# Optimization experiments

Hardware: AMD Instinct MI355X
Metric: run time of the kernel (lower is better)

The kernel has to match this reference:

```python
import jax, jax.numpy as jnp
import numpy as np

V = 500000        # total elements
S = 50000         # num samples (segments)
D = 128           # input = hidden = output size


def setup_inputs() -> dict:
    key = jax.random.key(0)
    k1, k2, k3, k4, k5 = jax.random.split(key, 5)
    scale = 1.0 / np.sqrt(D)
    return {
        "element_embeddings": jax.random.normal(k1, (V, D), dtype=jnp.float32),
        "element_to_sample_map": jnp.sort(jax.random.randint(k2, (V,), 0, S)),
        "num_samples": S,
        "Wq": jax.random.normal(k3, (D, D), dtype=jnp.float32) * scale,
        "Wk": jax.random.normal(k4, (D, D), dtype=jnp.float32) * scale,
        "Wo": jax.random.normal(k5, (D, D), dtype=jnp.float32) * scale,
    }


def reference(element_embeddings, element_to_sample_map, num_samples, Wq, Wk, Wo):
    x = element_embeddings                    # [V, D]
    idx = element_to_sample_map               # [V] int

    # --- query summarizer: linear projection + segment mean ---
    q_elem = x @ Wq.T                          # [V, H]
    q_sum = jax.ops.segment_sum(q_elem, idx, num_segments=num_samples)   # [S, H]
    counts = jax.ops.segment_sum(jnp.ones((x.shape[0],), x.dtype), idx,
                                 num_segments=num_samples)               # [S]
    queries = q_sum / jnp.maximum(counts, 1.0)[:, None]                  # [S, H]

    # --- attention scores: gather query per element, dot with key ---
    keys = x @ Wk.T                            # [V, H]
    queries_all = queries[idx]                 # [V, H] gather
    scores = jnp.einsum('vh,vh->v', queries_all, keys)                   # [V]

    # --- segment softmax (exp of scatter_log_softmax, eps=0) ---
    seg_max = jax.ops.segment_max(scores, idx, num_segments=num_samples) # [S]
    shifted = scores - seg_max[idx]
    e = jnp.exp(shifted)
    denom = jax.ops.segment_sum(e, idx, num_segments=num_samples)        # [S]
    probs = e / denom[idx]                                               # [V]

    # --- weighted scatter-sum of output projections ---
    out_elem = (x @ Wo.T) * probs[:, None]     # [V, D_out]
    return jax.ops.segment_sum(out_elem, idx, num_segments=num_samples)  # [S, D_out]
```

## Files before the change

kernel.cpp:

```cpp
#include <hip/hip_runtime.h>
#include <math.h>

#define D 128
#define RPW 64
#define WPB 4
#define RPB (RPW * WPB)

__global__ void k_prep(const float* __restrict__ Wq, const float* __restrict__ Wk,
                       const float* __restrict__ Wo, float* __restrict__ M,
                       float* __restrict__ WoT) {
  int j = blockIdx.x, k = threadIdx.x;
  float acc = 0.f;
#pragma unroll 8
  for (int i = 0; i < D; ++i) acc = fmaf(Wq[i * D + j], Wk[i * D + k], acc);
  M[j * D + k] = acc;
  WoT[j * D + k] = Wo[k * D + j];
}

__global__ void k_zero(float4* __restrict__ p, long long nf4) {
  long long i = (long long)blockIdx.x * blockDim.x + threadIdx.x;
  long long st = (long long)gridDim.x * blockDim.x;
  float4 z = make_float4(0.f, 0.f, 0.f, 0.f);
  for (; i < nf4; i += st) p[i] = z;
}

template <int PASS>
__global__ __launch_bounds__(256) void k_segsum(
    const float* __restrict__ x, const int* __restrict__ idx,
    const float* __restrict__ t, float* __restrict__ gout,
    float* __restrict__ gden, int V) {
  const int lane = threadIdx.x & 63;
  const int wave = threadIdx.x >> 6;
  const int r0 = blockIdx.x * RPB + wave * RPW;
  if (r0 >= V) return;

  const int myIdx = idx[min(r0 + lane, V - 1)];
  const int prevIdx = __shfl_up(myIdx, 1);
  const unsigned long long chg = __ballot(lane > 0 && myIdx != prevIdx);

  const float* xw = x + (size_t)r0 * D + lane * 2;
  float2 acc = make_float2(0.f, 0.f);
  float dacc = 0.f;
  int curSeg = __shfl(myIdx, 0);
  int runStart = 0;
  float2 t2 = make_float2(0.f, 0.f);
  if (PASS == 2) t2 = *(const float2*)(t + (size_t)curSeg * D + lane * 2);

#pragma unroll
  for (int c = 0; c < RPW / 8; ++c) {
    float2 xr[8];
#pragma unroll
    for (int j = 0; j < 8; ++j) {
      int rr = min(r0 + c * 8 + j, V - 1) - r0;
      xr[j] = *(const float2*)(xw + (size_t)rr * D);
    }
#pragma unroll
    for (int j = 0; j < 8; ++j) {
      const int i = c * 8 + j;
      const bool valid = (r0 + i) < V;
      if (i > 0 && ((chg >> i) & 1ull)) {
        float* gp = gout + (size_t)curSeg * D + lane * 2;
        if (runStart > 0) {
          gp[0] = acc.x;
          gp[1] = acc.y;
          if (lane == 0) gden[curSeg] = dacc;
        } else {
          unsafeAtomicAdd(gp + 0, acc.x);
          unsafeAtomicAdd(gp + 1, acc.y);
          if (lane == 0) unsafeAtomicAdd(gden + curSeg, dacc);
        }
        acc = make_float2(0.f, 0.f);
        dacc = 0.f;
        curSeg = __shfl(myIdx, i);
        runStart = i;
        if (PASS == 2) t2 = *(const float2*)(t + (size_t)curSeg * D + lane * 2);
      }
      float w;
      if (PASS == 1) {
        w = valid ? 1.f : 0.f;
      } else {
        float p = t2.x * xr[j].x + t2.y * xr[j].y;
        p += __shfl_xor(p, 32);
        p += __shfl_xor(p, 16);
        p += __shfl_xor(p, 8);
        p += __shfl_xor(p, 4);
        p += __shfl_xor(p, 2);
        p += __shfl_xor(p, 1);
        w = valid ? __expf(p) : 0.f;
      }
      acc.x = fmaf(w, xr[j].x, acc.x);
      acc.y = fmaf(w, xr[j].y, acc.y);
      dacc += w;
    }
  }
  float* gp = gout + (size_t)curSeg * D + lane * 2;
  unsafeAtomicAdd(gp + 0, acc.x);
  unsafeAtomicAdd(gp + 1, acc.y);
  if (lane == 0) unsafeAtomicAdd(gden + curSeg, dacc);
}

template <int MODE>
__global__ void k_rowmat4(const float* __restrict__ in, const float* __restrict__ B,
                          float* __restrict__ out, int S,
                          const float* __restrict__ den) {
  __shared__ float Bl[D * D];
  for (int i = threadIdx.x; i < D * D / 4; i += (int)blockDim.x)
    ((float4*)Bl)[i] = ((const float4*)B)[i];
  __syncthreads();
  int t = blockIdx.x * blockDim.x + threadIdx.x;
  int g = t & 31;
  int s0 = (t >> 5) * 4;
  if (s0 >= S) return;
  int nr = S - s0;
  nr = nr > 4 ? 4 : nr;
  float4 a0 = make_float4(0, 0, 0, 0), a1 = a0, a2 = a0, a3 = a0;
  const float4* r0 = (const float4*)(in + (size_t)s0 * D);
  const float4* r1 = (const float4*)(in + (size_t)(s0 + 1) * D);
  const float4* r2 = (const float4*)(in + (size_t)(s0 + 2) * D);
  const float4* r3 = (const float4*)(in + (size_t)(s0 + 3) * D);
#pragma unroll 4
  for (int j4 = 0; j4 < D / 4; ++j4) {
    float4 b0 = *(const float4*)(Bl + (j4 * 4 + 0) * D + g * 4);
    float4 b1 = *(const float4*)(Bl + (j4 * 4 + 1) * D + g * 4);
    float4 b2 = *(const float4*)(Bl + (j4 * 4 + 2) * D + g * 4);
    float4 b3 = *(const float4*)(Bl + (j4 * 4 + 3) * D + g * 4);
#define ROWFMA(ar, rr)                                                   \
    {                                                                    \
      float4 m = rr[j4];                                                 \
      ar.x = fmaf(m.x, b0.x, ar.x); ar.y = fmaf(m.x, b0.y, ar.y);        \
      ar.z = fmaf(m.x, b0.z, ar.z); ar.w = fmaf(m.x, b0.w, ar.w);        \
      ar.x = fmaf(m.y, b1.x, ar.x); ar.y = fmaf(m.y, b1.y, ar.y);        \
      ar.z = fmaf(m.y, b1.z, ar.z); ar.w = fmaf(m.y, b1.w, ar.w);        \
      ar.x = fmaf(m.z, b2.x, ar.x); ar.y = fmaf(m.z, b2.y, ar.y);        \
      ar.z = fmaf(m.z, b2.z, ar.z); ar.w = fmaf(m.z, b2.w, ar.w);        \
      ar.x = fmaf(m.w, b3.x, ar.x); ar.y = fmaf(m.w, b3.y, ar.y);        \
      ar.z = fmaf(m.w, b3.z, ar.z); ar.w = fmaf(m.w, b3.w, ar.w);        \
    }
    ROWFMA(a0, r0);
    if (nr > 1) ROWFMA(a1, r1);
    if (nr > 2) ROWFMA(a2, r2);
    if (nr > 3) ROWFMA(a3, r3);
#undef ROWFMA
  }
  float sc[4];
#pragma unroll
  for (int k = 0; k < 4; ++k) {
    int s = s0 + (k < nr ? k : 0);
    float dn = den[s];
    if (MODE == 0) sc[k] = 1.f / fmaxf(dn, 1.f);
    else sc[k] = (dn > 0.f) ? 1.f / dn : 0.f;
  }
  a0.x *= sc[0]; a0.y *= sc[0]; a0.z *= sc[0]; a0.w *= sc[0];
  a1.x *= sc[1]; a1.y *= sc[1]; a1.z *= sc[1]; a1.w *= sc[1];
  a2.x *= sc[2]; a2.y *= sc[2]; a2.z *= sc[2]; a2.w *= sc[2];
  a3.x *= sc[3]; a3.y *= sc[3]; a3.z *= sc[3]; a3.w *= sc[3];
  *(float4*)(out + (size_t)s0 * D + g * 4) = a0;
  if (nr > 1) *(float4*)(out + (size_t)(s0 + 1) * D + g * 4) = a1;
  if (nr > 2) *(float4*)(out + (size_t)(s0 + 2) * D + g * 4) = a2;
  if (nr > 3) *(float4*)(out + (size_t)(s0 + 3) * D + g * 4) = a3;
}

extern "C" void kernel_launch(void* const* d_in, const int* in_sizes, int n_in,
                              void* d_out, int out_size, void* d_ws, size_t ws_size,
                              hipStream_t stream) {
  const float* x = (const float*)d_in[0];
  const int* idx = (const int*)d_in[1];
  const float* Wq = (const float*)d_in[3];
  const float* Wk = (const float*)d_in[4];
  const float* Wo = (const float*)d_in[5];
  float* out = (float*)d_out;
  const int V = in_sizes[1];
  const int S = out_size / D;

  char* ws = (char*)d_ws;
  float* M = (float*)(ws + 0);
  float* WoT = (float*)(ws + 65536);
  size_t base = 131072;
  float* qsum = (float*)(ws + base);
  float* ysum = qsum + (size_t)S * D;
  float* cnt = ysum + (size_t)S * D;
  float* den = cnt + S;
  long long zf4 = ((long long)S * (2 * D + 2)) / 4;
  size_t tbase = (base + (size_t)S * (2 * D + 2) * 4 + 255) & ~(size_t)255;
  float* t = (float*)(ws + tbase);

  const int NT = (V + RPB - 1) / RPB;
  const int rmBlocks = ((S + 3) / 4 * 32 + 255) / 256;

  hipLaunchKernelGGL(k_prep, dim3(D), dim3(D), 0, stream, Wq, Wk, Wo, M, WoT);
  hipLaunchKernelGGL(k_zero, dim3(2048), dim3(256), 0, stream, (float4*)qsum, zf4);
  hipLaunchKernelGGL((k_segsum<1>), dim3(NT), dim3(256), 0, stream, x, idx,
                     (const float*)nullptr, qsum, cnt, V);
  hipLaunchKernelGGL((k_rowmat4<0>), dim3(rmBlocks), dim3(256), 0, stream, qsum, M, t, S, cnt);
  hipLaunchKernelGGL((k_segsum<2>), dim3(NT), dim3(256), 0, stream, x, idx, t, ysum, den, V);
  hipLaunchKernelGGL((k_rowmat4<1>), dim3(rmBlocks), dim3(256), 0, stream, ysum, WoT, out, S, den);
}
```

Measured before the change: 298.1 us.

## Fuse all stages into one persistent kernel with software grid barriers

Replaces six kernel launches with a single persistent kernel sized from occupancy. Its phases (zero/prep, pass-1 segment sum, query projection, pass-2 weighted sum, output projection) are separated by an atomic sense-reversing grid barrier. The aim is to remove launch gaps and tail effects between the small stages. The segment passes now use 32-row waves in grid-strided tiles, and the rowmat phase stages B in 32-row chunks through a smaller shared buffer. The software barrier relies on all blocks being co-resident, which plain launches do not guarantee, and it adds spin overhead and smaller per-wave work.

```diff
diff --git a/kernel.cpp b/kernel.cpp
--- a/kernel.cpp
+++ b/kernel.cpp
@@ -2,162 +2,243 @@
 #include <math.h>
 
 #define D 128
-#define RPW 64
-#define WPB 4
-#define RPB (RPW * WPB)
-
-__global__ void k_prep(const float* __restrict__ Wq, const float* __restrict__ Wk,
-                       const float* __restrict__ Wo, float* __restrict__ M,
-                       float* __restrict__ WoT) {
-  int j = blockIdx.x, k = threadIdx.x;
-  float acc = 0.f;
-#pragma unroll 8
-  for (int i = 0; i < D; ++i) acc = fmaf(Wq[i * D + j], Wk[i * D + k], acc);
-  M[j * D + k] = acc;
-  WoT[j * D + k] = Wo[k * D + j];
-}
-
-__global__ void k_zero(float4* __restrict__ p, long long nf4) {
-  long long i = (long long)blockIdx.x * blockDim.x + threadIdx.x;
-  long long st = (long long)gridDim.x * blockDim.x;
-  float4 z = make_float4(0.f, 0.f, 0.f, 0.f);
-  for (; i < nf4; i += st) p[i] = z;
+#define TPB 512
+#define WPB 8
+#define RPWAVE 32
+#define RPT (WPB * RPWAVE)
+
+__device__ __forceinline__ void grid_barrier(int* gcount, int* gsense, int nb,
+                                             int* bsense) {
+  __syncthreads();
+  if (threadIdx.x == 0) {
+    int s = 1 - *bsense;
+    *bsense = s;
+    __threadfence();
+    int arrived = __hip_atomic_fetch_add(gcount, 1, __ATOMIC_ACQ_REL,
+                                         __HIP_MEMORY_SCOPE_AGENT);
+    if (arrived == nb - 1) {
+      __hip_atomic_store(gcount, 0, __ATOMIC_RELAXED, __HIP_MEMORY_SCOPE_AGENT);
+      __hip_atomic_store(gsense, s, __ATOMIC_RELEASE, __HIP_MEMORY_SCOPE_AGENT);
+    } else {
+      while (__hip_atomic_load(gsense, __ATOMIC_ACQUIRE,
+                               __HIP_MEMORY_SCOPE_AGENT) != s)
+        __builtin_amdgcn_s_sleep(8);
+    }
+  }
+  __syncthreads();
 }
 
 template <int PASS>
-__global__ __launch_bounds__(256) void k_segsum(
-    const float* __restrict__ x, const int* __restrict__ idx,
-    const float* __restrict__ t, float* __restrict__ gout,
-    float* __restrict__ gden, int V) {
+__device__ __forceinline__ void seg_pass(const float* __restrict__ x,
+                                         const int* __restrict__ idx,
+                                         const float* __restrict__ t,
+                                         float* __restrict__ gout,
+                                         float* __restrict__ gden, int V) {
   const int lane = threadIdx.x & 63;
   const int wave = threadIdx.x >> 6;
-  const int r0 = blockIdx.x * RPB + wave * RPW;
-  if (r0 >= V) return;
-
-  const int myIdx = idx[min(r0 + lane, V - 1)];
-  const int prevIdx = __shfl_up(myIdx, 1);
-  const unsigned long long chg = __ballot(lane > 0 && myIdx != prevIdx);
-
-  const float* xw = x + (size_t)r0 * D + lane * 2;
-  float2 acc = make_float2(0.f, 0.f);
-  float dacc = 0.f;
-  int curSeg = __shfl(myIdx, 0);
-  int runStart = 0;
-  float2 t2 = make_float2(0.f, 0.f);
-  if (PASS == 2) t2 = *(const float2*)(t + (size_t)curSeg * D + lane * 2);
-
-#pragma unroll
-  for (int c = 0; c < RPW / 8; ++c) {
-    float2 xr[8];
-#pragma unroll
-    for (int j = 0; j < 8; ++j) {
-      int rr = min(r0 + c * 8 + j, V - 1) - r0;
-      xr[j] = *(const float2*)(xw + (size_t)rr * D);
-    }
-#pragma unroll
-    for (int j = 0; j < 8; ++j) {
-      const int i = c * 8 + j;
-      const bool valid = (r0 + i) < V;
-      if (i > 0 && ((chg >> i) & 1ull)) {
-        float* gp = gout + (size_t)curSeg * D + lane * 2;
-        if (runStart > 0) {
-          gp[0] = acc.x;
-          gp[1] = acc.y;
-          if (lane == 0) gden[curSeg] = dacc;
+  const int NT = (V + RPT - 1) / RPT;
+  for (int tile = blockIdx.x; tile < NT; tile += gridDim.x) {
+    const int r0 = tile * RPT + wave * RPWAVE;
+    if (r0 >= V) continue;
+    int rowIdx = idx[min(r0 + (lane & 31), V - 1)];
+    int prev = __shfl_up(rowIdx, 1);
+    unsigned long long chg = __ballot(lane > 0 && lane < 32 && rowIdx != prev);
+
+    float2 acc = make_float2(0.f, 0.f);
+    float dacc = 0.f;
+    int curSeg = __shfl(rowIdx, 0);
+    int runStart = 0;
+    float2 t2 = make_float2(0.f, 0.f);
+    if (PASS == 2) t2 = *(const float2*)(t + (size_t)curSeg * D + lane * 2);
+
+#pragma unroll
+    for (int c = 0; c < RPWAVE / 8; ++c) {
+      float2 xr[8];
+#pragma unroll
+      for (int j = 0; j < 8; ++j) {
+        int row = r0 + c * 8 + j;
+        row = row < V ? row : V - 1;
+        xr[j] = *(const float2*)(x + (size_t)row * D + lane * 2);
+      }
+#pragma unroll
+      for (int j = 0; j < 8; ++j) {
+        const int i = c * 8 + j;
+        const bool valid = (r0 + i) < V;
+        if (i > 0 && ((chg >> i) & 1ull)) {
+          float* gp = gout + (size_t)curSeg * D + lane * 2;
+          if (runStart > 0) {
+            gp[0] = acc.x;
+            gp[1] = acc.y;
+            if (lane == 0) gden[curSeg] = dacc;
+          } else {
+            unsafeAtomicAdd(gp + 0, acc.x);
+            unsafeAtomicAdd(gp + 1, acc.y);
+            if (lane == 0) unsafeAtomicAdd(gden + curSeg, dacc);
+          }
+          acc = make_float2(0.f, 0.f);
+          dacc = 0.f;
+          curSeg = __shfl(rowIdx, i);
+          runStart = i;
+          if (PASS == 2) t2 = *(const float2*)(t + (size_t)curSeg * D + lane * 2);
+        }
+        float w;
+        if (PASS == 1) {
+          w = valid ? 1.f : 0.f;
         } else {
-          unsafeAtomicAdd(gp + 0, acc.x);
-          unsafeAtomicAdd(gp + 1, acc.y);
-          if (lane == 0) unsafeAtomicAdd(gden + curSeg, dacc);
-        }
-        acc = make_float2(0.f, 0.f);
-        dacc = 0.f;
-        curSeg = __shfl(myIdx, i);
-        runStart = i;
-        if (PASS == 2) t2 = *(const float2*)(t + (size_t)curSeg * D + lane * 2);
-      }
-      float w;
-      if (PASS == 1) {
-        w = valid ? 1.f : 0.f;
-      } else {
-        float p = t2.x * xr[j].x + t2.y * xr[j].y;
-        p += __shfl_xor(p, 32);
-        p += __shfl_xor(p, 16);
-        p += __shfl_xor(p, 8);
-        p += __shfl_xor(p, 4);
-        p += __shfl_xor(p, 2);
-        p += __shfl_xor(p, 1);
-        w = valid ? __expf(p) : 0.f;
-      }
-      acc.x = fmaf(w, xr[j].x, acc.x);
-      acc.y = fmaf(w, xr[j].y, acc.y);
-      dacc += w;
-    }
-  }
-  float* gp = gout + (size_t)curSeg * D + lane * 2;
-  unsafeAtomicAdd(gp + 0, acc.x);
-  unsafeAtomicAdd(gp + 1, acc.y);
-  if (lane == 0) unsafeAtomicAdd(gden + curSeg, dacc);
-}
+          float p = t2.x * xr[j].x + t2.y * xr[j].y;
+          p += __shfl_xor(p, 32);
+          p += __shfl_xor(p, 16);
+          p += __shfl_xor(p, 8);
+          p += __shfl_xor(p, 4);
+          p += __shfl_xor(p, 2);
+          p += __shfl_xor(p, 1);
+          w = valid ? __expf(p) : 0.f;
+        }
+        acc.x = fmaf(w, xr[j].x, acc.x);
+        acc.y = fmaf(w, xr[j].y, acc.y);
+        dacc += w;
+      }
+    }
+    float* gp = gout + (size_t)curSeg * D + lane * 2;
+    unsafeAtomicAdd(gp + 0, acc.x);
+    unsafeAtomicAdd(gp + 1, acc.y);
+    if (lane == 0) unsafeAtomicAdd(gden + curSeg, dacc);
+  }
+}
+
+#define FMA16(ar, m, b0, b1, b2, b3)                                   \
+  {                                                                    \
+    ar.x = fmaf(m.x, b0.x, ar.x); ar.y = fmaf(m.x, b0.y, ar.y);        \
+    ar.z = fmaf(m.x, b0.z, ar.z); ar.w = fmaf(m.x, b0.w, ar.w);        \
+    ar.x = fmaf(m.y, b1.x, ar.x); ar.y = fmaf(m.y, b1.y, ar.y);        \
+    ar.z = fmaf(m.y, b1.z, ar.z); ar.w = fmaf(m.y, b1.w, ar.w);        \
+    ar.x = fmaf(m.z, b2.x, ar.x); ar.y = fmaf(m.z, b2.y, ar.y);        \
+    ar.z = fmaf(m.z, b2.z, ar.z); ar.w = fmaf(m.z, b2.w, ar.w);        \
+    ar.x = fmaf(m.w, b3.x, ar.x); ar.y = fmaf(m.w, b3.y, ar.y);        \
+    ar.z = fmaf(m.w, b3.z, ar.z); ar.w = fmaf(m.w, b3.w, ar.w);        \
+  }
 
 template <int MODE>
-__global__ void k_rowmat4(const float* __restrict__ in, const float* __restrict__ B,
-                          float* __restrict__ out, int S,
-                          const float* __restrict__ den) {
-  __shared__ float Bl[D * D];
-  for (int i = threadIdx.x; i < D * D / 4; i += (int)blockDim.x)
-    ((float4*)Bl)[i] = ((const float4*)B)[i];
-  __syncthreads();
-  int t = blockIdx.x * blockDim.x + threadIdx.x;
-  int g = t & 31;
-  int s0 = (t >> 5) * 4;
-  if (s0 >= S) return;
-  int nr = S - s0;
-  nr = nr > 4 ? 4 : nr;
-  float4 a0 = make_float4(0, 0, 0, 0), a1 = a0, a2 = a0, a3 = a0;
-  const float4* r0 = (const float4*)(in + (size_t)s0 * D);
-  const float4* r1 = (const float4*)(in + (size_t)(s0 + 1) * D);
-  const float4* r2 = (const float4*)(in + (size_t)(s0 + 2) * D);
-  const float4* r3 = (const float4*)(in + (size_t)(s0 + 3) * D);
-#pragma unroll 4
-  for (int j4 = 0; j4 < D / 4; ++j4) {
-    float4 b0 = *(const float4*)(Bl + (j4 * 4 + 0) * D + g * 4);
-    float4 b1 = *(const float4*)(Bl + (j4 * 4 + 1) * D + g * 4);
-    float4 b2 = *(const float4*)(Bl + (j4 * 4 + 2) * D + g * 4);
-    float4 b3 = *(const float4*)(Bl + (j4 * 4 + 3) * D + g * 4);
-#define ROWFMA(ar, rr)                                                   \
-    {                                                                    \
-      float4 m = rr[j4];                                                 \
-      ar.x = fmaf(m.x, b0.x, ar.x); ar.y = fmaf(m.x, b0.y, ar.y);        \
-      ar.z = fmaf(m.x, b0.z, ar.z); ar.w = fmaf(m.x, b0.w, ar.w);        \
-      ar.x = fmaf(m.y, b1.x, ar.x); ar.y = fmaf(m.y, b1.y, ar.y);        \
-      ar.z = fmaf(m.y, b1.z, ar.z); ar.w = fmaf(m.y, b1.w, ar.w);        \
-      ar.x = fmaf(m.z, b2.x, ar.x); ar.y = fmaf(m.z, b2.y, ar.y);        \
-      ar.z = fmaf(m.z, b2.z, ar.z); ar.w = fmaf(m.z, b2.w, ar.w);        \
-      ar.x = fmaf(m.w, b3.x, ar.x); ar.y = fmaf(m.w, b3.y, ar.y);        \
-      ar.z = fmaf(m.w, b3.z, ar.z); ar.w = fmaf(m.w, b3.w, ar.w);        \
-    }
-    ROWFMA(a0, r0);
-    if (nr > 1) ROWFMA(a1, r1);
-    if (nr > 2) ROWFMA(a2, r2);
-    if (nr > 3) ROWFMA(a3, r3);
-#undef ROWFMA
-  }
-  float sc[4];
-#pragma unroll
-  for (int k = 0; k < 4; ++k) {
-    int s = s0 + (k < nr ? k : 0);
-    float dn = den[s];
-    if (MODE == 0) sc[k] = 1.f / fmaxf(dn, 1.f);
-    else sc[k] = (dn > 0.f) ? 1.f / dn : 0.f;
-  }
-  a0.x *= sc[0]; a0.y *= sc[0]; a0.z *= sc[0]; a0.w *= sc[0];
-  a1.x *= sc[1]; a1.y *= sc[1]; a1.z *= sc[1]; a1.w *= sc[1];
-  a2.x *= sc[2]; a2.y *= sc[2]; a2.z *= sc[2]; a2.w *= sc[2];
-  a3.x *= sc[3]; a3.y *= sc[3]; a3.z *= sc[3]; a3.w *= sc[3];
-  *(float4*)(out + (size_t)s0 * D + g * 4) = a0;
-  if (nr > 1) *(float4*)(out + (size_t)(s0 + 1) * D + g * 4) = a1;
-  if (nr > 2) *(float4*)(out + (size_t)(s0 + 2) * D + g * 4) = a2;
-  if (nr > 3) *(float4*)(out + (size_t)(s0 + 3) * D + g * 4) = a3;
+__device__ __forceinline__ void rowmat_phase(const float* __restrict__ in,
+                                             const float* __restrict__ B,
+                                             float* __restrict__ outp,
+                                             const float* __restrict__ scale_src,
+                                             int S, float* Bl) {
+  const int tid = threadIdx.x;
+  const int g = tid & 31;
+  const int gl = tid >> 5;
+  const int NG = (S + 127) / 128;
+  for (int bt = blockIdx.x; bt < NG; bt += gridDim.x) {
+    const int gid0 = bt * 32 + gl;
+    const int gid1 = bt * 32 + 16 + gl;
+    float4 accA[4], accB[4];
+#pragma unroll
+    for (int r = 0; r < 4; ++r) {
+      accA[r] = make_float4(0.f, 0.f, 0.f, 0.f);
+      accB[r] = make_float4(0.f, 0.f, 0.f, 0.f);
+    }
+#pragma unroll
+    for (int c = 0; c < 4; ++c) {
+      __syncthreads();
+#pragma unroll
+      for (int u = 0; u < 2; ++u) {
+        int e = tid + u * TPB;
+        ((float4*)Bl)[e] = ((const float4*)(B + 32 * c * D))[e];
+      }
+      __syncthreads();
+#pragma unroll
+      for (int jj4 = 0; jj4 < 8; ++jj4) {
+        float4 b0 = *(const float4*)(Bl + (jj4 * 4 + 0) * D + g * 4);
+        float4 b1 = *(const float4*)(Bl + (jj4 * 4 + 1) * D + g * 4);
+        float4 b2 = *(const float4*)(Bl + (jj4 * 4 + 2) * D + g * 4);
+        float4 b3 = *(const float4*)(Bl + (jj4 * 4 + 3) * D + g * 4);
+#pragma unroll
+        for (int r = 0; r < 4; ++r) {
+          int s = gid0 * 4 + r;
+          if (s < S) {
+            float4 m = *(const float4*)(in + (size_t)s * D + c * 32 + jj4 * 4);
+            FMA16(accA[r], m, b0, b1, b2, b3);
+          }
+        }
+#pragma unroll
+        for (int r = 0; r < 4; ++r) {
+          int s = gid1 * 4 + r;
+          if (s < S) {
+            float4 m = *(const float4*)(in + (size_t)s * D + c * 32 + jj4 * 4);
+            FMA16(accB[r], m, b0, b1, b2, b3);
+          }
+        }
+      }
+    }
+#pragma unroll
+    for (int r = 0; r < 4; ++r) {
+      int s = gid0 * 4 + r;
+      if (s < S) {
+        float dn = scale_src[s];
+        float sc = (MODE == 0) ? 1.f / fmaxf(dn, 1.f) : ((dn > 0.f) ? 1.f / dn : 0.f);
+        float4 a = accA[r];
+        a.x *= sc; a.y *= sc; a.z *= sc; a.w *= sc;
+        *(float4*)(outp + (size_t)s * D + g * 4) = a;
+      }
+    }
+#pragma unroll
+    for (int r = 0; r < 4; ++r) {
+      int s = gid1 * 4 + r;
+      if (s < S) {
+        float dn = scale_src[s];
+        float sc = (MODE == 0) ? 1.f / fmaxf(dn, 1.f) : ((dn > 0.f) ? 1.f / dn : 0.f);
+        float4 a = accB[r];
+        a.x *= sc; a.y *= sc; a.z *= sc; a.w *= sc;
+        *(float4*)(outp + (size_t)s * D + g * 4) = a;
+      }
+    }
+  }
+}
+
+__global__ __launch_bounds__(TPB, 4) void k_all(
+    const float* __restrict__ x, const int* __restrict__ idx,
+    const float* __restrict__ Wq, const float* __restrict__ Wk,
+    const float* __restrict__ Wo, float* __restrict__ M, float* __restrict__ WoT,
+    float* __restrict__ qsum, float* __restrict__ ysum, float* __restrict__ cnt,
+    float* __restrict__ den, float* __restrict__ t, float* __restrict__ out,
+    int* gbar, int V, int S) {
+  __shared__ float Bl[32 * D];
+  __shared__ int bsense;
+  if (threadIdx.x == 0) bsense = 0;
+  const int nb = gridDim.x;
+  const int tid = threadIdx.x;
+
+  {
+    long long zf4 = ((long long)S * (2 * D + 2)) / 4;
+    float4 z = make_float4(0.f, 0.f, 0.f, 0.f);
+    for (long long i = (long long)blockIdx.x * TPB + tid; i < zf4;
+         i += (long long)nb * TPB)
+      ((float4*)qsum)[i] = z;
+    if (blockIdx.x < 32) {
+      int j = blockIdx.x * 4 + (tid >> 7);
+      int k = tid & 127;
+      float a = 0.f;
+#pragma unroll 8
+      for (int i = 0; i < D; ++i) a = fmaf(Wq[i * D + j], Wk[i * D + k], a);
+      M[j * D + k] = a;
+    } else if (blockIdx.x < 64) {
+      int e = (blockIdx.x - 32) * TPB + tid;
+      int j = e >> 7, k = e & 127;
+      WoT[j * D + k] = Wo[k * D + j];
+    }
+  }
+  grid_barrier(gbar, gbar + 1, nb, &bsense);
+
+  seg_pass<1>(x, idx, (const float*)nullptr, qsum, cnt, V);
+  grid_barrier(gbar, gbar + 1, nb, &bsense);
+
+  rowmat_phase<0>(qsum, M, t, cnt, S, Bl);
+  grid_barrier(gbar, gbar + 1, nb, &bsense);
+
+  seg_pass<2>(x, idx, t, ysum, den, V);
+  grid_barrier(gbar, gbar + 1, nb, &bsense);
+
+  rowmat_phase<1>(ysum, WoT, out, den, S, Bl);
 }
 
 extern "C" void kernel_launch(void* const* d_in, const int* in_sizes, int n_in,
@@ -175,23 +256,22 @@
   char* ws = (char*)d_ws;
   float* M = (float*)(ws + 0);
   float* WoT = (float*)(ws + 65536);
-  size_t base = 131072;
+  int* gbar = (int*)(ws + 131072);
+  size_t base = 131072 + 256;
   float* qsum = (float*)(ws + base);
   float* ysum = qsum + (size_t)S * D;
   float* cnt = ysum + (size_t)S * D;
   float* den = cnt + S;
-  long long zf4 = ((long long)S * (2 * D + 2)) / 4;
-  size_t tbase = (base + (size_t)S * (2 * D + 2) * 4 + 255) & ~(size_t)255;
-  float* t = (float*)(ws + tbase);
-
-  const int NT = (V + RPB - 1) / RPB;
-  const int rmBlocks = ((S + 3) / 4 * 32 + 255) / 256;
-
-  hipLaunchKernelGGL(k_prep, dim3(D), dim3(D), 0, stream, Wq, Wk, Wo, M, WoT);
-  hipLaunchKernelGGL(k_zero, dim3(2048), dim3(256), 0, stream, (float4*)qsum, zf4);
-  hipLaunchKernelGGL((k_segsum<1>), dim3(NT), dim3(256), 0, stream, x, idx,
-                     (const float*)nullptr, qsum, cnt, V);
-  hipLaunchKernelGGL((k_rowmat4<0>), dim3(rmBlocks), dim3(256), 0, stream, qsum, M, t, S, cnt);
-  hipLaunchKernelGGL((k_segsum<2>), dim3(NT), dim3(256), 0, stream, x, idx, t, ysum, den, V);
-  hipLaunchKernelGGL((k_rowmat4<1>), dim3(rmBlocks), dim3(256), 0, stream, ysum, WoT, out, S, den);
-}
+  float* t = den + S;
+
+  int blocksPerCU = 0;
+  hipOccupancyMaxActiveBlocksPerMultiprocessor(&blocksPerCU, k_all, TPB, 0);
+  if (blocksPerCU < 1) blocksPerCU = 1;
+  long long nb_ll = (long long)blocksPerCU * 256;
+  int nb = (int)(nb_ll > 1024 ? 1024 : nb_ll);
+  if (nb < 256) nb = 256;
+
+  hipMemsetAsync(gbar, 0, 8, stream);
+  hipLaunchKernelGGL(k_all, dim3(nb), dim3(TPB), 0, stream, x, idx, Wq, Wk, Wo,
+                     M, WoT, qsum, ysum, cnt, den, t, out, gbar, V, S);
+}
```

Result: slower. 539.2 us (+80.9%).
